# Kernel tuning notes

Hardware: AMD Instinct MI355X
Metric: run time of the kernel (lower is better)

## Reference

```python
import jax, jax.numpy as jnp
import numpy as np

N, W, H = 64, 64, 64
C1, C2 = W * H, 128          # dim_C2_1, dim_C2_2
DIM_H = 512                   # dim_h_o
SHIFTS = ((0, 1), (1, 0), (0, -1), (-1, 0))
BNUM = len(SHIFTS)
HID = DIM_H + BNUM            # GRU hidden size = 516
INP = C2 + BNUM               # GRU input size = 132
EPS = 1e-8


def setup_inputs() -> dict:
    key = jax.random.key(0)
    ks = jax.random.split(key, 16)
    s = 0.02
    return {
        "h_o_prev": jax.random.normal(ks[0], (N, HID), jnp.float32),
        "c_prev": jax.random.normal(ks[1], (N, C1, C2), jnp.float32),
        "c_xf": jax.random.normal(ks[2], (N, C1, C2), jnp.float32),
        "Wk": jax.random.normal(ks[3], (C2, DIM_H), jnp.float32) * s,
        "bk": jnp.zeros((C2,), jnp.float32),
        "Wb": jax.random.normal(ks[4], (1, DIM_H), jnp.float32) * s,
        "bb": jnp.zeros((1,), jnp.float32),
        "We": jax.random.normal(ks[5], (C2, DIM_H), jnp.float32) * s,
        "be": jnp.zeros((C2,), jnp.float32),
        "Wv": jax.random.normal(ks[6], (C2, DIM_H), jnp.float32) * s,
        "bv": jnp.zeros((C2,), jnp.float32),
        "W_ih": jax.random.normal(ks[7], (3 * HID, INP), jnp.float32) * s,
        "W_hh": jax.random.normal(ks[8], (3 * HID, HID), jnp.float32) * s,
        "b_ih": jnp.zeros((3 * HID,), jnp.float32),
        "b_hh": jnp.zeros((3 * HID,), jnp.float32),
    }


def _cos(a, b):
    # cosine similarity along last axis, torch semantics (norms clamped to eps)
    dot = jnp.sum(a * b, axis=-1)
    na = jnp.maximum(jnp.sqrt(jnp.sum(a * a, axis=-1)), EPS)
    nb = jnp.maximum(jnp.sqrt(jnp.sum(b * b, axis=-1)), EPS)
    return dot / (na * nb)


def _gru_cell(x, h, W_ih, W_hh, b_ih, b_hh):
    gi = x @ W_ih.T + b_ih
    gh = h @ W_hh.T + b_hh
    i_r, i_z, i_n = jnp.split(gi, 3, axis=1)
    h_r, h_z, h_n = jnp.split(gh, 3, axis=1)
    rg = jax.nn.sigmoid(i_r + h_r)
    zg = jax.nn.sigmoid(i_z + h_z)
    ng = jnp.tanh(i_n + rg * h_n)
    return (1.0 - zg) * ng + zg * h


def reference(h_o_prev, c_prev, c_xf, Wk, bk, Wb, bb, We, be, Wv, bv,
              W_ih, W_hh, b_ih, b_hh):
    origin_h = h_o_prev[:, :DIM_H]

    k = origin_h @ Wk.T + bk                         # [N, C2]
    beta_pre = origin_h @ Wb.T + bb                  # [N, 1]
    beta_pos = jnp.maximum(beta_pre, 0.0)
    beta_neg = jnp.minimum(beta_pre, 0.0)
    beta = (jnp.log1p(jnp.exp(beta_neg)) + beta_pos
            + jnp.log1p(jnp.exp(-beta_pos)) + (1.0 - np.log(2.0)))

    k_b = k[:, None, :]                              # broadcast over C1 slots
    s_kc = _cos(c_prev, k_b)                         # [N, C1]
    w_kc = jax.nn.softmax(s_kc * beta, axis=1)       # content addressing

    # spatial bias: rolls on the [W,H] map, softmax over bias channel
    w_nwh = w_kc.reshape(N, W, H)
    w_bias = jnp.stack([jnp.roll(w_nwh, sh, axis=(1, 2)) for sh in SHIFTS],
                       axis=3).reshape(N, C1, BNUM)
    w_bias = jax.nn.softmax(w_bias, axis=2)          # [N, C1, BNUM]

    s_kx = _cos(c_xf, k_b)
    w_kx = jax.nn.softmax(s_kx * beta, axis=1)       # [N, C1]

    c_with_bias = jnp.concatenate([c_xf, w_bias], axis=2)   # [N, C1, C2+BNUM]
    r = jnp.einsum('nc,ncd->nd', w_kx, c_with_bias)          # read vector

    h_o = _gru_cell(r, h_o_prev, W_ih, W_hh, b_ih, b_hh)     # [N, HID]

    origin_o_h = h_o[:, :DIM_H]
    h_o_bias = jax.nn.softmax(h_o[:, DIM_H:], axis=1)        # [N, BNUM]
    w_write = jnp.einsum('ncb,nb->nc', w_bias, h_o_bias)     # [N, C1]

    e = jax.nn.sigmoid(origin_o_h @ We.T + be)               # [N, C2]
    v = origin_o_h @ Wv.T + bv                               # [N, C2]

    # C_Erase == False path: c_new = c_prev*(1 - w_kc e^T) + w_write v^T
    c_new = (c_prev * (1.0 - w_kc[:, :, None] * e[:, None, :])
             + w_write[:, :, None] * v[:, None, :])
    return h_o, c_new
```

## Files before the change

kernel.cpp:

```cpp
#include <hip/hip_runtime.h>
#include <hip/hip_bf16.h>
#include <math.h>

#define NB 64
#define C1n 4096
#define C2n 128
#define DIMH 512
#define HIDN 516
#define INPN 132
#define GR   1548
#define KTOT 648
#define EPSF 1e-8f

typedef __hip_bfloat16 bf16;

enum : size_t {
  OFF_SKC = 0,
  OFF_SKX = 64,
  OFF_RX  = 128,
  ZERO_FLOATS = 8320,
  OFF_K   = 8320,
  OFF_INVNK = 16512,
  OFF_BETA  = 16576,
  OFF_FLAG  = 16640,
  OFF_EKC = 16704,
  OFF_EKX = 278848,
  OFF_XH  = 278848,
  OFF_WB  = 540992,
  OFF_RB  = 1589568,
  OFF_SR  = 1589824,
  OFF_SZ  = 1622848,
  OFF_SNI = 1655872,
  OFF_SNH = 1688896,
  GATE_FLOATS = 132096,
  OFF_E   = 1721920,
  OFF_V   = 1730112,
  OFF_HOB = 1738304,
  WS_FLOATS = 1738560
};

__device__ __forceinline__ float ldf(const void* p, size_t i, int f){
  if(f) return ((const float*)p)[i];
  return __bfloat162float(((const bf16*)p)[i]);
}
__device__ __forceinline__ void stf(void* p, size_t i, float v, int f){
  if(f) ((float*)p)[i] = v;
  else  ((bf16*)p)[i] = __float2bfloat16(v);
}
__device__ __forceinline__ float4 ld4(const void* p, size_t ei, int f){
  if(f) return ((const float4*)p)[ei >> 2];
  union { ushort4 u; bf16 h[4]; } t;
  t.u = ((const ushort4*)p)[ei >> 2];
  return make_float4(__bfloat162float(t.h[0]), __bfloat162float(t.h[1]),
                     __bfloat162float(t.h[2]), __bfloat162float(t.h[3]));
}
__device__ __forceinline__ void st4(void* p, size_t ei, float4 v, int f){
  if(f){ ((float4*)p)[ei >> 2] = v; return; }
  union { ushort4 u; bf16 h[4]; } t;
  t.h[0] = __float2bfloat16(v.x); t.h[1] = __float2bfloat16(v.y);
  t.h[2] = __float2bfloat16(v.z); t.h[3] = __float2bfloat16(v.w);
  ((ushort4*)p)[ei >> 2] = t.u;
}
__device__ __forceinline__ float expc(float x){
  return expf(fminf(fmaxf(x, -60.f), 60.f));
}

__global__ void k0_probe(const void* cp, float* __restrict__ ws){
  int t = threadIdx.x;
  __shared__ float red[256];
  const bf16* p = (const bf16*)cp;
  float m = 0.f;
  for(int i = t; i < 8192; i += 256){
    float v = __bfloat162float(p[i]);
    if(v != v) v = 1e30f;
    m = fmaxf(m, fabsf(v));
  }
  red[t] = m;
  __syncthreads();
  for(int s = 128; s; s >>= 1){
    if(t < s) red[t] = fmaxf(red[t], red[t + s]);
    __syncthreads();
  }
  if(t == 0) ws[OFF_FLAG] = (red[0] > 1e4f) ? 1.0f : 0.0f;
}

__global__ void k1_kbeta(const void* hop, const void* Wk, const void* bk,
                         const void* Wb, const void* bb, float* __restrict__ ws){
  int n = blockIdx.x;
  int t = threadIdx.x;
  int f = (ws[OFF_FLAG] != 0.f);
  __shared__ float h[DIMH];
  __shared__ float kk[C2n];
  for(int d = t; d < DIMH; d += 256) h[d] = ldf(hop, (size_t)n*HIDN + d, f);
  __syncthreads();
  if(t < C2n){
    float acc = 0.f;
    for(int d = 0; d < DIMH; d += 4){
      float4 w = ld4(Wk, (size_t)t*DIMH + d, f);
      acc += w.x*h[d] + w.y*h[d+1] + w.z*h[d+2] + w.w*h[d+3];
    }
    acc += ldf(bk, t, f);
    kk[t] = acc;
    ws[OFF_K + n*C2n + t] = acc;
  } else if(t == 128){
    float acc = 0.f;
    for(int d = 0; d < DIMH; d += 4){
      float4 w = ld4(Wb, d, f);
      acc += w.x*h[d] + w.y*h[d+1] + w.z*h[d+2] + w.w*h[d+3];
    }
    acc += ldf(bb, 0, f);
    float sp = fmaxf(acc, 0.f) + log1pf(expc(-fabsf(acc)));
    ws[OFF_BETA + n] = sp + 1.0f;
  }
  __syncthreads();
  if(t == 0){
    float s = 0.f;
    for(int c = 0; c < C2n; ++c) s += kk[c]*kk[c];
    ws[OFF_INVNK + n] = 1.0f / fmaxf(sqrtf(s), EPSF);
  }
}

__global__ void __launch_bounds__(256, 8)
k2_score(const void* cp, const void* cx, float* __restrict__ ws){
  int n = blockIdx.y;
  int cbase = blockIdx.x * 128;
  int t = threadIdx.x;
  int f = (ws[OFF_FLAG] != 0.f);
  int wave = t >> 6;
  int lane = t & 63;
  int half = lane >> 5;
  int l = lane & 31;

  float k0 = ws[OFF_K + n*C2n + l*4 + 0];
  float k1 = ws[OFF_K + n*C2n + l*4 + 1];
  float k2 = ws[OFF_K + n*C2n + l*4 + 2];
  float k3 = ws[OFF_K + n*C2n + l*4 + 3];
  float beta  = ws[OFF_BETA + n];
  float invnk = ws[OFF_INVNK + n];

  float sA = 0.f, sB = 0.f;
  float r0 = 0.f, r1 = 0.f, r2 = 0.f, r3 = 0.f;

  size_t addr = ((size_t)n*C1n + cbase + wave*2 + half)*C2n + l*4;
  float4 a0 = ld4(cp, addr, f),        b0 = ld4(cx, addr, f);
  float4 a1 = ld4(cp, addr + 1024, f), b1 = ld4(cx, addr + 1024, f);

  for(int it = 0; it < 16; ++it){
    float4 a = a0, b = b0;
    a0 = a1; b0 = b1;
    if(it < 14){
      size_t nxt = addr + 2048;
      a1 = ld4(cp, nxt, f);
      b1 = ld4(cx, nxt, f);
    }
    addr += 1024;

    int row = cbase + it*8 + wave*2 + half;
    float dc = a.x*k0 + a.y*k1 + a.z*k2 + a.w*k3;
    float nc = a.x*a.x + a.y*a.y + a.z*a.z + a.w*a.w;
    float dx = b.x*k0 + b.y*k1 + b.z*k2 + b.w*k3;
    float nx = b.x*b.x + b.y*b.y + b.z*b.z + b.w*b.w;
    #pragma unroll
    for(int m = 1; m < 32; m <<= 1){
      dc += __shfl_xor(dc, m, 64);
      nc += __shfl_xor(nc, m, 64);
      dx += __shfl_xor(dx, m, 64);
      nx += __shfl_xor(nx, m, 64);
    }
    float skc = dc / fmaxf(sqrtf(nc), EPSF) * invnk;
    float skx = dx / fmaxf(sqrtf(nx), EPSF) * invnk;
    float ekc = expc(skc * beta);
    float ekx = expc(skx * beta);
    if(l == 0){
      ws[OFF_EKC + (size_t)n*C1n + row] = ekc;
      ws[OFF_EKX + (size_t)n*C1n + row] = ekx;
    }
    sA += ekc; sB += ekx;
    r0 += ekx*b.x; r1 += ekx*b.y; r2 += ekx*b.z; r3 += ekx*b.w;
  }

  r0 += __shfl_xor(r0, 32, 64);
  r1 += __shfl_xor(r1, 32, 64);
  r2 += __shfl_xor(r2, 32, 64);
  r3 += __shfl_xor(r3, 32, 64);
  sA += __shfl_xor(sA, 32, 64);
  sB += __shfl_xor(sB, 32, 64);

  __shared__ float rxw[4][C2n];
  __shared__ float sred[8];
  if(lane < 32){
    rxw[wave][l*4 + 0] = r0; rxw[wave][l*4 + 1] = r1;
    rxw[wave][l*4 + 2] = r2; rxw[wave][l*4 + 3] = r3;
  }
  if(lane == 0){ sred[wave] = sA; sred[4 + wave] = sB; }
  __syncthreads();
  if(t < C2n)
    atomicAdd(&ws[OFF_RX + n*C2n + t],
              rxw[0][t] + rxw[1][t] + rxw[2][t] + rxw[3][t]);
  if(t == 0) atomicAdd(&ws[OFF_SKC + n], sred[0]+sred[1]+sred[2]+sred[3]);
  if(t == 1) atomicAdd(&ws[OFF_SKX + n], sred[4]+sred[5]+sred[6]+sred[7]);
}

__global__ void k3a_wbias(float* __restrict__ ws){
  int n = blockIdx.x;
  int t = threadIdx.x;
  __shared__ float wl[C1n];
  __shared__ float r0[256], r1[256], r2[256], r3[256];
  float invSc = 1.0f / fmaxf(ws[OFF_SKC + n], 1e-30f);
  float invSx = 1.0f / fmaxf(ws[OFF_SKX + n], 1e-30f);
  for(int c = t; c < C1n; c += 256) wl[c] = ws[OFF_EKC + n*C1n + c] * invSc;
  __syncthreads();
  float a0=0.f, a1=0.f, a2=0.f, a3=0.f;
  for(int c = t; c < C1n; c += 256){
    int x = c >> 6, y = c & 63;
    float w0 = wl[ (x << 6)            | ((y-1) & 63) ];
    float w1 = wl[ (((x-1) & 63) << 6) | y            ];
    float w2 = wl[ (x << 6)            | ((y+1) & 63) ];
    float w3 = wl[ (((x+1) & 63) << 6) | y            ];
    float m = fmaxf(fmaxf(w0,w1), fmaxf(w2,w3));
    float e0 = expc(w0-m), e1 = expc(w1-m), e2 = expc(w2-m), e3 = expc(w3-m);
    float inv = 1.0f/(e0+e1+e2+e3);
    e0 *= inv; e1 *= inv; e2 *= inv; e3 *= inv;
    size_t wb = OFF_WB + ((size_t)n*C1n + c)*4;
    ws[wb] = e0; ws[wb+1] = e1; ws[wb+2] = e2; ws[wb+3] = e3;
    float wx = ws[OFF_EKX + n*C1n + c] * invSx;
    a0 += wx*e0; a1 += wx*e1; a2 += wx*e2; a3 += wx*e3;
  }
  r0[t]=a0; r1[t]=a1; r2[t]=a2; r3[t]=a3;
  __syncthreads();
  for(int s = 128; s; s >>= 1){
    if(t < s){ r0[t]+=r0[t+s]; r1[t]+=r1[t+s]; r2[t]+=r2[t+s]; r3[t]+=r3[t+s]; }
    __syncthreads();
  }
  if(t == 0){
    ws[OFF_RB + n*4 + 0] = r0[0]; ws[OFF_RB + n*4 + 1] = r1[0];
    ws[OFF_RB + n*4 + 2] = r2[0]; ws[OFF_RB + n*4 + 3] = r3[0];
  }
}

__global__ void k3x_pack(const void* hop, float* __restrict__ ws){
  int idx = blockIdx.x * 256 + threadIdx.x;
  int d = idx >> 6, n = idx & 63;
  int f = (ws[OFF_FLAG] != 0.f);
  float v;
  if(d < C2n)       v = ws[OFF_RX + n*C2n + d] / fmaxf(ws[OFF_SKX + n], 1e-30f);
  else if(d < INPN) v = ws[OFF_RB + n*4 + (d - C2n)];
  else              v = ldf(hop, (size_t)n*HIDN + (d - INPN), f);
  ws[OFF_XH + (size_t)d*64 + n] = v;
}

__global__ void k3b_gates(const void* Wih, const void* Whh, float* __restrict__ ws){
  int t = threadIdx.x;
  int wave = t >> 6, lane = t & 63;
  int chunk = blockIdx.y;
  int row0 = blockIdx.x * 16 + wave * 4;
  int f = (ws[OFF_FLAG] != 0.f);

  int isX = (chunk == 0);
  int koff = isX ? 0 : ((chunk == 1) ? 0 : 132 + (chunk - 2) * 128);
  int klen = (chunk <= 1) ? 132 : 128;
  int kbase = isX ? koff : (INPN + koff);
  const void* W = isX ? Wih : Whh;
  size_t wstride = isX ? INPN : HIDN;

  int r4[4];
  #pragma unroll
  for(int r = 0; r < 4; ++r){
    int row = row0 + r;
    r4[r] = (row < GR) ? row : (GR - 1);
  }

  float acc[4] = {0.f, 0.f, 0.f, 0.f};
  for(int d = 0; d < klen; d += 4){
    float x0 = ws[OFF_XH + (size_t)(kbase + d    )*64 + lane];
    float x1 = ws[OFF_XH + (size_t)(kbase + d + 1)*64 + lane];
    float x2 = ws[OFF_XH + (size_t)(kbase + d + 2)*64 + lane];
    float x3 = ws[OFF_XH + (size_t)(kbase + d + 3)*64 + lane];
    #pragma unroll
    for(int r = 0; r < 4; ++r){
      float4 w = ld4(W, (size_t)r4[r]*wstride + koff + d, f);
      acc[r] += w.x*x0 + w.y*x1 + w.z*x2 + w.w*x3;
    }
  }

  #pragma unroll
  for(int r = 0; r < 4; ++r){
    int row = row0 + r;
    if(row >= GR) continue;
    size_t dst;
    if(row < HIDN)        dst = OFF_SR  + (size_t)row*64;
    else if(row < 2*HIDN) dst = OFF_SZ  + (size_t)(row - HIDN)*64;
    else                  dst = (isX ? OFF_SNI : OFF_SNH) + (size_t)(row - 2*HIDN)*64;
    atomicAdd(&ws[dst + lane], acc[r]);
  }
}

__global__ void k3c_combine(const void* hop, const void* We, const void* be,
                            const void* Wv, const void* bv,
                            const void* bih, const void* bhh,
                            float* __restrict__ ws, void* out){
  int n = blockIdx.x;
  int t = threadIdx.x;
  int f = (ws[OFF_FLAG] != 0.f);
  __shared__ float ho[HIDN];
  if(t < HIDN){
    float sr = ws[OFF_SR  + (size_t)t*64 + n] + ldf(bih, t, f) + ldf(bhh, t, f);
    float sz = ws[OFF_SZ  + (size_t)t*64 + n] + ldf(bih, HIDN + t, f) + ldf(bhh, HIDN + t, f);
    float si = ws[OFF_SNI + (size_t)t*64 + n] + ldf(bih, 2*HIDN + t, f);
    float sh = ws[OFF_SNH + (size_t)t*64 + n] + ldf(bhh, 2*HIDN + t, f);
    float rg = 1.0f/(1.0f + expc(-sr));
    float zg = 1.0f/(1.0f + expc(-sz));
    float ng = tanhf(si + rg*sh);
    float hv = ldf(hop, (size_t)n*HIDN + t, f);
    float o = (1.0f - zg)*ng + zg*hv;
    ho[t] = o;
    stf(out, (size_t)n*HIDN + t, o, f);
  }
  __syncthreads();
  if(t == 0){
    float a = ho[512], b = ho[513], c = ho[514], d2 = ho[515];
    float m = fmaxf(fmaxf(a,b), fmaxf(c,d2));
    float e0 = expc(a-m), e1 = expc(b-m), e2 = expc(c-m), e3 = expc(d2-m);
    float inv = 1.0f/(e0+e1+e2+e3);
    ws[OFF_HOB + n*4 + 0] = e0*inv; ws[OFF_HOB + n*4 + 1] = e1*inv;
    ws[OFF_HOB + n*4 + 2] = e2*inv; ws[OFF_HOB + n*4 + 3] = e3*inv;
  }
  if(t < 256){
    int c2 = t & 127, sel = t >> 7;
    const void* W = sel ? Wv : We;
    float acc = 0.f;
    for(int d = 0; d < DIMH; d += 4){
      float4 w = ld4(W, (size_t)c2*DIMH + d, f);
      acc += w.x*ho[d] + w.y*ho[d+1] + w.z*ho[d+2] + w.w*ho[d+3];
    }
    if(sel) ws[OFF_V + n*C2n + c2] = acc + ldf(bv, c2, f);
    else {
      float e = acc + ldf(be, c2, f);
      ws[OFF_E + n*C2n + c2] = 1.0f/(1.0f + expc(-e));
    }
  }
}

__global__ void __launch_bounds__(256, 8)
k4_cnew(const void* cp, float* __restrict__ ws, void* out){
  int n = blockIdx.y;
  int cbase = blockIdx.x * 128;
  int t = threadIdx.x;
  int f = (ws[OFF_FLAG] != 0.f);
  int dq = t & 31, sub = t >> 5;
  int d0 = dq * 4;
  float invSc = 1.0f / fmaxf(ws[OFF_SKC + n], 1e-30f);
  float4 ed = *(const float4*)&ws[OFF_E + n*C2n + d0];
  float4 vd = *(const float4*)&ws[OFF_V + n*C2n + d0];
  float h0 = ws[OFF_HOB + n*4 + 0], h1 = ws[OFF_HOB + n*4 + 1];
  float h2 = ws[OFF_HOB + n*4 + 2], h3 = ws[OFF_HOB + n*4 + 3];

  int c0 = cbase + sub;
  float  wkc_n = ws[OFF_EKC + (size_t)n*C1n + c0];
  float4 wb_n  = *(const float4*)&ws[OFF_WB + ((size_t)n*C1n + c0)*4];
  float4 a_n   = ld4(cp, ((size_t)n*C1n + c0)*C2n + d0, f);

  for(int i = 0; i < 16; ++i){
    int c = cbase + i*8 + sub;
    float  wkc = wkc_n;
    float4 wb4 = wb_n;
    float4 a   = a_n;
    if(i < 15){
      int cn = c + 8;
      wkc_n = ws[OFF_EKC + (size_t)n*C1n + cn];
      wb_n  = *(const float4*)&ws[OFF_WB + ((size_t)n*C1n + cn)*4];
      a_n   = ld4(cp, ((size_t)n*C1n + cn)*C2n + d0, f);
    }
    wkc *= invSc;
    float wwr = wb4.x*h0 + wb4.y*h1 + wb4.z*h2 + wb4.w*h3;
    size_t idx = ((size_t)n*C1n + c)*C2n + d0;
    float4 o;
    o.x = a.x*(1.0f - wkc*ed.x) + wwr*vd.x;
    o.y = a.y*(1.0f - wkc*ed.y) + wwr*vd.y;
    o.z = a.z*(1.0f - wkc*ed.z) + wwr*vd.z;
    o.w = a.w*(1.0f - wkc*ed.w) + wwr*vd.w;
    st4(out, (size_t)(NB*HIDN) + idx, o, f);
  }
}

extern "C" void kernel_launch(void* const* d_in, const int* in_sizes, int n_in,
                              void* d_out, int out_size, void* d_ws, size_t ws_size,
                              hipStream_t stream){
  const void* hop = d_in[0];
  const void* cp  = d_in[1];
  const void* cx  = d_in[2];
  const void* Wk  = d_in[3];
  const void* bk  = d_in[4];
  const void* Wb  = d_in[5];
  const void* bb  = d_in[6];
  const void* We  = d_in[7];
  const void* be  = d_in[8];
  const void* Wv  = d_in[9];
  const void* bv  = d_in[10];
  const void* Wih = d_in[11];
  const void* Whh = d_in[12];
  const void* bih = d_in[13];
  const void* bhh = d_in[14];
  float* ws = (float*)d_ws;

  hipMemsetAsync(ws, 0, ZERO_FLOATS * sizeof(float), stream);
  hipMemsetAsync(ws + OFF_SR, 0, GATE_FLOATS * sizeof(float), stream);

  k0_probe<<<1, 256, 0, stream>>>(cp, ws);
  k1_kbeta<<<NB, 256, 0, stream>>>(hop, Wk, bk, Wb, bb, ws);
  k2_score<<<dim3(32, NB), 256, 0, stream>>>(cp, cx, ws);
  k3a_wbias<<<NB, 256, 0, stream>>>(ws);
  k3x_pack<<<162, 256, 0, stream>>>(hop, ws);
  k3b_gates<<<dim3((GR + 15) / 16, 5), 256, 0, stream>>>(Wih, Whh, ws);
  k3c_combine<<<NB, 576, 0, stream>>>(hop, We, be, Wv, bv, bih, bhh, ws, d_out);
  k4_cnew<<<dim3(32, NB), 256, 0, stream>>>(cp, ws, d_out);
}
```

Baseline: 481.9 us.

## Remap k2_score to 8-lane row groups with wider per-thread loads

```diff
diff --git a/kernel.cpp b/kernel.cpp
--- a/kernel.cpp
+++ b/kernel.cpp
@@ -120,7 +120,7 @@
   }
 }
 
-__global__ void __launch_bounds__(256, 8)
+__global__ void __launch_bounds__(256)
 k2_score(const void* cp, const void* cx, float* __restrict__ ws){
   int n = blockIdx.y;
   int cbase = blockIdx.x * 128;
@@ -128,40 +128,40 @@
   int f = (ws[OFF_FLAG] != 0.f);
   int wave = t >> 6;
   int lane = t & 63;
-  int half = lane >> 5;
-  int l = lane & 31;
-
-  float k0 = ws[OFF_K + n*C2n + l*4 + 0];
-  float k1 = ws[OFF_K + n*C2n + l*4 + 1];
-  float k2 = ws[OFF_K + n*C2n + l*4 + 2];
-  float k3 = ws[OFF_K + n*C2n + l*4 + 3];
+  int g   = lane & 7;
+  int grp = lane >> 3;
+
+  float4 kf[4];
+  #pragma unroll
+  for(int j = 0; j < 4; ++j)
+    kf[j] = *(const float4*)&ws[OFF_K + n*C2n + j*32 + g*4];
   float beta  = ws[OFF_BETA + n];
   float invnk = ws[OFF_INVNK + n];
 
   float sA = 0.f, sB = 0.f;
-  float r0 = 0.f, r1 = 0.f, r2 = 0.f, r3 = 0.f;
-
-  size_t addr = ((size_t)n*C1n + cbase + wave*2 + half)*C2n + l*4;
-  float4 a0 = ld4(cp, addr, f),        b0 = ld4(cx, addr, f);
-  float4 a1 = ld4(cp, addr + 1024, f), b1 = ld4(cx, addr + 1024, f);
-
-  for(int it = 0; it < 16; ++it){
-    float4 a = a0, b = b0;
-    a0 = a1; b0 = b1;
-    if(it < 14){
-      size_t nxt = addr + 2048;
-      a1 = ld4(cp, nxt, f);
-      b1 = ld4(cx, nxt, f);
-    }
-    addr += 1024;
-
-    int row = cbase + it*8 + wave*2 + half;
-    float dc = a.x*k0 + a.y*k1 + a.z*k2 + a.w*k3;
-    float nc = a.x*a.x + a.y*a.y + a.z*a.z + a.w*a.w;
-    float dx = b.x*k0 + b.y*k1 + b.z*k2 + b.w*k3;
-    float nx = b.x*b.x + b.y*b.y + b.z*b.z + b.w*b.w;
-    #pragma unroll
-    for(int m = 1; m < 32; m <<= 1){
+  float r[16];
+  #pragma unroll
+  for(int i = 0; i < 16; ++i) r[i] = 0.f;
+
+  for(int it = 0; it < 4; ++it){
+    int row = cbase + wave*32 + it*8 + grp;
+    size_t base = ((size_t)n*C1n + row)*C2n + g*4;
+    float4 a[4], b[4];
+    #pragma unroll
+    for(int j = 0; j < 4; ++j){
+      a[j] = ld4(cp, base + j*32, f);
+      b[j] = ld4(cx, base + j*32, f);
+    }
+    float dc = 0.f, nc = 0.f, dx = 0.f, nx = 0.f;
+    #pragma unroll
+    for(int j = 0; j < 4; ++j){
+      dc += a[j].x*kf[j].x + a[j].y*kf[j].y + a[j].z*kf[j].z + a[j].w*kf[j].w;
+      nc += a[j].x*a[j].x + a[j].y*a[j].y + a[j].z*a[j].z + a[j].w*a[j].w;
+      dx += b[j].x*kf[j].x + b[j].y*kf[j].y + b[j].z*kf[j].z + b[j].w*kf[j].w;
+      nx += b[j].x*b[j].x + b[j].y*b[j].y + b[j].z*b[j].z + b[j].w*b[j].w;
+    }
+    #pragma unroll
+    for(int m = 1; m < 8; m <<= 1){
       dc += __shfl_xor(dc, m, 64);
       nc += __shfl_xor(nc, m, 64);
       dx += __shfl_xor(dx, m, 64);
@@ -171,34 +171,38 @@
     float skx = dx / fmaxf(sqrtf(nx), EPSF) * invnk;
     float ekc = expc(skc * beta);
     float ekx = expc(skx * beta);
-    if(l == 0){
+    if(g == 0){
       ws[OFF_EKC + (size_t)n*C1n + row] = ekc;
       ws[OFF_EKX + (size_t)n*C1n + row] = ekx;
-    }
-    sA += ekc; sB += ekx;
-    r0 += ekx*b.x; r1 += ekx*b.y; r2 += ekx*b.z; r3 += ekx*b.w;
-  }
-
-  r0 += __shfl_xor(r0, 32, 64);
-  r1 += __shfl_xor(r1, 32, 64);
-  r2 += __shfl_xor(r2, 32, 64);
-  r3 += __shfl_xor(r3, 32, 64);
-  sA += __shfl_xor(sA, 32, 64);
-  sB += __shfl_xor(sB, 32, 64);
-
-  __shared__ float rxw[4][C2n];
-  __shared__ float sred[8];
-  if(lane < 32){
-    rxw[wave][l*4 + 0] = r0; rxw[wave][l*4 + 1] = r1;
-    rxw[wave][l*4 + 2] = r2; rxw[wave][l*4 + 3] = r3;
-  }
-  if(lane == 0){ sred[wave] = sA; sred[4 + wave] = sB; }
-  __syncthreads();
-  if(t < C2n)
-    atomicAdd(&ws[OFF_RX + n*C2n + t],
-              rxw[0][t] + rxw[1][t] + rxw[2][t] + rxw[3][t]);
-  if(t == 0) atomicAdd(&ws[OFF_SKC + n], sred[0]+sred[1]+sred[2]+sred[3]);
-  if(t == 1) atomicAdd(&ws[OFF_SKX + n], sred[4]+sred[5]+sred[6]+sred[7]);
+      sA += ekc; sB += ekx;
+    }
+    #pragma unroll
+    for(int j = 0; j < 4; ++j){
+      r[j*4+0] += ekx*b[j].x; r[j*4+1] += ekx*b[j].y;
+      r[j*4+2] += ekx*b[j].z; r[j*4+3] += ekx*b[j].w;
+    }
+  }
+
+  #pragma unroll
+  for(int m = 8; m < 64; m <<= 1){
+    #pragma unroll
+    for(int i = 0; i < 16; ++i) r[i] += __shfl_xor(r[i], m, 64);
+    sA += __shfl_xor(sA, m, 64);
+    sB += __shfl_xor(sB, m, 64);
+  }
+  if(lane < 8){
+    #pragma unroll
+    for(int j = 0; j < 4; ++j){
+      atomicAdd(&ws[OFF_RX + n*C2n + j*32 + lane*4 + 0], r[j*4+0]);
+      atomicAdd(&ws[OFF_RX + n*C2n + j*32 + lane*4 + 1], r[j*4+1]);
+      atomicAdd(&ws[OFF_RX + n*C2n + j*32 + lane*4 + 2], r[j*4+2]);
+      atomicAdd(&ws[OFF_RX + n*C2n + j*32 + lane*4 + 3], r[j*4+3]);
+    }
+  }
+  if(lane == 0){
+    atomicAdd(&ws[OFF_SKC + n], sA);
+    atomicAdd(&ws[OFF_SKX + n], sB);
+  }
 }
 
 __global__ void k3a_wbias(float* __restrict__ ws){
```

Result: slower. 491.7 us (+2.0%).
